# Optimization experiments

Hardware: AMD Instinct MI355X
Metric: run time of the kernel (lower is better)

The kernel has to match this reference:

```python
import jax, jax.numpy as jnp
import numpy as np

IO = 1024
D_SLOT = 128
SCALES = [1, 2, 4]
N = 4          # lcm of scales (streams / period)
K = 3          # number of scales (active slots per step)
S = 7          # sum of scales (total slots)
D = D_SLOT * S # 896, per-stream dim
H = K * N      # 12 heads
RANK = 256
HID = 3584
B, T = 4, 1024
EPS = 1e-5


def _tables():
    # active_slots[phase, scale_idx] -> slot id
    act = np.zeros((N, K), dtype=np.int32)
    for p in range(N):
        off = 0
        for i, s in enumerate(SCALES):
            act[p, i] = off + p % s
            off += s
    # head_assignments[stream, slot] -> head id (SHARED mode)
    ha = np.zeros((N, S), dtype=np.int32)
    off = 0
    for i, s in enumerate(SCALES):
        alpha = N // s
        for j in range(s):
            ha[:, off + j] = i * N + (np.arange(N) + alpha * j) % N
        off += s
    return act, ha

ACTIVE_SLOTS, HEAD_ASSIGN = _tables()


def layernorm(x, g, b):
    m = jnp.mean(x, axis=-1, keepdims=True)
    v = jnp.mean(jnp.square(x - m), axis=-1, keepdims=True)
    return (x - m) * jax.lax.rsqrt(v + EPS) * g + b


def setup_inputs() -> dict:
    key = jax.random.key(0)
    ks = jax.random.split(key, 16)
    f32 = jnp.float32
    return {
        'x': jax.random.normal(ks[0], (B, T, IO), f32),
        't': 3,
        'enc_base_w': jax.random.normal(ks[1], (D, IO), f32) * 0.02,
        'enc_A_w': jax.random.normal(ks[2], (RANK, IO), f32) * 0.02,
        'enc_B': jax.random.normal(ks[3], (RANK, N, D), f32) * 0.02,
        'enc_beta': jnp.asarray(0.01, f32),
        'ln_mixer_g': jnp.ones((D,), f32),
        'ln_mixer_b': jnp.zeros((D,), f32),
        'mix_w1': jax.random.normal(ks[4], (HID, D), f32) * 0.02,
        'mix_b1': jnp.zeros((HID,), f32),
        'mix_w2': jax.random.normal(ks[5], (D, HID), f32) * 0.02,
        'mix_b2': jnp.zeros((D,), f32),
        'ln_attn_g': jnp.ones((D,), f32),
        'ln_attn_b': jnp.zeros((D,), f32),
        'Wq': jax.random.normal(ks[6], (H, D, D_SLOT), f32) * 0.02,
        'Wk': jax.random.normal(ks[7], (H, D, D_SLOT), f32) * 0.02,
        'Wv': jax.random.normal(ks[8], (H, D, D_SLOT), f32) * 0.02,
        'dec_ln_g': jnp.ones((N * D,), f32),
        'dec_ln_b': jnp.zeros((N * D,), f32),
        'dec_down_w': jax.random.normal(ks[9], (RANK, N * D), f32) * 0.02,
        'dec_up_w': jax.random.normal(ks[10], (IO, RANK), f32) * 0.02,
    }


def reference(x, t, enc_base_w, enc_A_w, enc_B, enc_beta,
              ln_mixer_g, ln_mixer_b, mix_w1, mix_b1, mix_w2, mix_b2,
              ln_attn_g, ln_attn_b, Wq, Wk, Wv,
              dec_ln_g, dec_ln_b, dec_down_w, dec_up_w):
    b, tt, _ = x.shape
    # --- StreamLoRAEncoder: x [B,T,IO] -> z [B,T,N,D] ---
    base = x @ enc_base_w.T                       # [B,T,D]
    h = x @ enc_A_w.T                             # [B,T,RANK]
    delta = jnp.einsum('btr,rnd->btnd', h, enc_B) # [B,T,N,D]
    z = base[:, :, None, :] + enc_beta * delta

    # --- step(z, t, is_causal=True) ---
    phase = int(t) % N
    active = ACTIVE_SLOTS[phase]                               # [K]
    head_ids = HEAD_ASSIGN[np.arange(N)[:, None], active[None, :]]  # [N,K]

    # mixer (pre-LN MLP residual)
    zm = layernorm(z, ln_mixer_g, ln_mixer_b)
    m = jax.nn.gelu(zm @ mix_w1.T + mix_b1, approximate=False) @ mix_w2.T + mix_b2
    z_head = z + m                                             # [B,T,N,D]

    # per-head multi-scale attention; head input scope = STREAM (full D)
    hin = layernorm(z_head, ln_attn_g, ln_attn_b)              # [B,T,N,D]
    Wq_s, Wk_s, Wv_s = Wq[head_ids], Wk[head_ids], Wv[head_ids]  # [N,K,D,d]
    q = jnp.einsum('btnc,nkcd->btnkd', hin, Wq_s)
    k = jnp.einsum('btnc,nkcd->btnkd', hin, Wk_s)
    v = jnp.einsum('btnc,nkcd->btnkd', hin, Wv_s)
    scale = 1.0 / jnp.sqrt(jnp.asarray(D_SLOT, q.dtype))
    scores = jnp.einsum('bqnkd,bpnkd->bnkqp', q, k) * scale    # [B,N,K,T,T]
    causal = jnp.tril(jnp.ones((tt, tt), dtype=bool))
    scores = jnp.where(causal, scores, jnp.finfo(scores.dtype).min)
    attn = jax.nn.softmax(scores, axis=-1)
    out = jnp.einsum('bnkqp,bpnkd->bqnkd', attn, v)            # [B,T,N,K,d]

    # write attention outputs back into the active slots (residual)
    z_slots = z_head.reshape(b, tt, N, S, D_SLOT)
    z_new = z_slots.at[:, :, :, jnp.asarray(active), :].add(out)
    z_new = z_new.reshape(b, tt, N, D)

    # --- StreamLoRADecoder: z [B,T,N,D] -> y [B,T,IO] ---
    cat = z_new.reshape(b, tt, N * D)
    c = layernorm(cat, dec_ln_g, dec_ln_b)
    y = (c @ dec_down_w.T) @ dec_up_w.T
    return y
```

## Files before the change

### kernel.cpp

```cpp
#include <hip/hip_runtime.h>
#include <hip/hip_bf16.h>
#include <math.h>

typedef __hip_bfloat16 bf16;
typedef __attribute__((ext_vector_type(8))) short v8s;
typedef __attribute__((ext_vector_type(4))) float v4f;

#define EPI_F32    0
#define EPI_BF16   1
#define EPI_GELU   2
#define EPI_RESID  3
#define EPI_BCAST4 4
#define EPI_AXPY   5
#define EPI_RESID0 6

__device__ __forceinline__ float bf_lo(unsigned int w) { return __uint_as_float(w << 16); }
__device__ __forceinline__ float bf_hi(unsigned int w) { return __uint_as_float(w & 0xffff0000u); }
__device__ __forceinline__ unsigned short f2b_bits(float f) {
  unsigned int u = __float_as_uint(f);
  unsigned int r = (u + 0x7fffu + ((u >> 16) & 1u)) >> 16;
  return (unsigned short)r;
}
__device__ __forceinline__ void unpack8(uint4 u, float* f) {
  unsigned int w0 = u.x, w1 = u.y, w2 = u.z, w3 = u.w;
  f[0] = bf_lo(w0); f[1] = bf_hi(w0);
  f[2] = bf_lo(w1); f[3] = bf_hi(w1);
  f[4] = bf_lo(w2); f[5] = bf_hi(w2);
  f[6] = bf_lo(w3); f[7] = bf_hi(w3);
}
__device__ __forceinline__ void load8(const float* p, float* f) {
  float4 a = ((const float4*)p)[0];
  float4 b = ((const float4*)p)[1];
  f[0] = a.x; f[1] = a.y; f[2] = a.z; f[3] = a.w;
  f[4] = b.x; f[5] = b.y; f[6] = b.z; f[7] = b.w;
}

__global__ __launch_bounds__(256) void cvt_kernel(const float* __restrict__ src,
                                                  bf16* __restrict__ dst, int n)
{
  int i = (blockIdx.x * 256 + threadIdx.x) * 8;
  if (i >= n) return;
  float f[8]; load8(src + i, f);
  unsigned short us[8];
#pragma unroll
  for (int j = 0; j < 8; j++) us[j] = f2b_bits(f[j]);
  *(uint4*)((unsigned short*)dst + i) = *(uint4*)us;
}

__global__ __launch_bounds__(256) void cvt_t_kernel(const float* __restrict__ src,
                                                    bf16* __restrict__ dst, int R, int C)
{
  __shared__ float tile[32][33];
  const int c0 = blockIdx.x * 32, r0 = blockIdx.y * 32;
  const size_t bo = (size_t)blockIdx.z * R * C;
  const int tx = threadIdx.x & 31, ty = threadIdx.x >> 5;
#pragma unroll
  for (int i = 0; i < 4; i++) {
    int r = ty * 4 + i;
    tile[r][tx] = src[bo + (size_t)(r0 + r) * C + c0 + tx];
  }
  __syncthreads();
#pragma unroll
  for (int i = 0; i < 4; i++) {
    int r = ty * 4 + i;
    *((unsigned short*)dst + bo + (size_t)(c0 + r) * R + r0 + tx) = f2b_bits(tile[tx][r]);
  }
}

__global__ __launch_bounds__(256) void vt_kernel(const bf16* __restrict__ v,
                                                 bf16* __restrict__ vt)
{
  __shared__ float tile[64][65];
  const int h = blockIdx.z;
  const int t0 = blockIdx.x * 64, d0 = blockIdx.y * 64;
  const bf16* src = v + (size_t)h * 4096 * 128;
  bf16* dst = vt + (size_t)h * 128 * 4096;
  const int tid = threadIdx.x;
#pragma unroll
  for (int tt = 0; tt < 2; tt++) {
    int s = tt * 256 + tid;
    int r = s >> 3, c0 = (s & 7) * 8;
    float f[8];
    uint4 u = *(const uint4*)(src + (size_t)(t0 + r) * 128 + d0 + c0);
    unpack8(u, f);
#pragma unroll
    for (int j = 0; j < 8; j++) tile[r][c0 + j] = f[j];
  }
  __syncthreads();
#pragma unroll
  for (int tt = 0; tt < 2; tt++) {
    int s = tt * 256 + tid;
    int dr = s >> 3, c0 = (s & 7) * 8;
    unsigned short us[8];
#pragma unroll
    for (int j = 0; j < 8; j++) us[j] = f2b_bits(tile[c0 + j][dr]);
    *(uint4*)((unsigned short*)dst + (size_t)(d0 + dr) * 4096 + t0 + c0) = *(uint4*)us;
  }
}

__device__ __forceinline__ void stage_tile(const bf16* __restrict__ src, int ld, int r0, int k0,
                                           bf16* lds, int tid)
{
#pragma unroll
  for (int t = 0; t < 2; t++) {
    int s = t * 256 + tid;
    int m = s >> 2, c = s & 3;
    uint4 u = *(const uint4*)(src + (size_t)(r0 + m) * ld + k0 + c * 8);
    *(uint4*)&lds[m * 40 + c * 8] = u;
  }
}
__device__ __forceinline__ void stage_tile(const float* __restrict__ src, int ld, int r0, int k0,
                                           bf16* lds, int tid)
{
#pragma unroll
  for (int t = 0; t < 2; t++) {
    int s = t * 256 + tid;
    int m = s >> 2, c = s & 3;
    float f[8]; load8(src + (size_t)(r0 + m) * ld + k0 + c * 8, f);
    unsigned short us[8];
#pragma unroll
    for (int j = 0; j < 8; j++) us[j] = f2b_bits(f[j]);
    *(uint4*)&lds[m * 40 + c * 8] = *(uint4*)us;
  }
}

template<typename TA, typename TB, int EPI>
__device__ void mfma_core(const TA* __restrict__ A, int lda,
                          const TB* __restrict__ B, int ldb,
                          void* __restrict__ C, int ldc,
                          const float* __restrict__ bias,
                          const float* __restrict__ beta_p,
                          int m0, int n0, int K)
{
  __shared__ bf16 As[128 * 40];
  __shared__ bf16 Bs[128 * 40];
  const int tid = threadIdx.x;
  const int lane = tid & 63, wave = tid >> 6;
  const int mw = (wave & 1) * 64, nw = (wave >> 1) * 64;
  const int row = lane & 15, kc = lane >> 4;

  v4f acc[4][4];
  const v4f vzero = {0.f, 0.f, 0.f, 0.f};
#pragma unroll
  for (int i = 0; i < 4; i++)
#pragma unroll
    for (int j = 0; j < 4; j++) acc[i][j] = vzero;

  for (int k0 = 0; k0 < K; k0 += 32) {
    stage_tile(A, lda, m0, k0, As, tid);
    stage_tile(B, ldb, n0, k0, Bs, tid);
    __syncthreads();
    v8s af[4], bfr[4];
#pragma unroll
    for (int i = 0; i < 4; i++)
      af[i] = *(const v8s*)&As[(mw + i * 16 + row) * 40 + kc * 8];
#pragma unroll
    for (int j = 0; j < 4; j++)
      bfr[j] = *(const v8s*)&Bs[(nw + j * 16 + row) * 40 + kc * 8];
#pragma unroll
    for (int i = 0; i < 4; i++)
#pragma unroll
      for (int j = 0; j < 4; j++)
        acc[i][j] = __builtin_amdgcn_mfma_f32_16x16x32_bf16(af[i], bfr[j], acc[i][j], 0, 0, 0);
    __syncthreads();
  }

  const int cl = lane & 15, rq = lane >> 4;
  const float beta = (EPI == EPI_AXPY) ? beta_p[0] : 0.f;
#pragma unroll
  for (int mi = 0; mi < 4; mi++) {
#pragma unroll
    for (int nj = 0; nj < 4; nj++) {
      const int col = n0 + nw + nj * 16 + cl;
#pragma unroll
      for (int i = 0; i < 4; i++) {
        const int r = m0 + mw + mi * 16 + rq * 4 + i;
        float v = acc[mi][nj][i];
        if (EPI == EPI_F32) {
          ((float*)C)[(size_t)r * ldc + col] = v;
        } else if (EPI == EPI_BF16) {
          ((unsigned short*)C)[(size_t)r * ldc + col] = f2b_bits(v);
        } else if (EPI == EPI_GELU) {
          v += bias[col];
          v = 0.5f * v * (1.f + erff(v * 0.70710678118654752f));
          ((unsigned short*)C)[(size_t)r * ldc + col] = f2b_bits(v);
        } else if (EPI == EPI_RESID) {
          float* Z = (float*)C;
          size_t idx = (size_t)r * ldc + col;
          Z[idx] = Z[idx] + v + bias[col];
        } else if (EPI == EPI_RESID0) {
          float* Z = (float*)C;
          size_t idx = (size_t)r * ldc + col;
          Z[idx] = Z[idx] + v;
        } else if (EPI == EPI_BCAST4) {
          float* Z = (float*)C;
#pragma unroll
          for (int rep = 0; rep < 4; rep++)
            Z[(size_t)r * 3584 + rep * 896 + col] = v;
        } else if (EPI == EPI_AXPY) {
          float* Z = (float*)C;
          size_t idx = (size_t)r * 3584 + col;
          Z[idx] = Z[idx] + beta * v;
        }
      }
    }
  }
}

template<typename TA, typename TB, int EPI>
__global__ __launch_bounds__(256) void mfma_gemm(const TA* __restrict__ A, int lda,
                                                 const TB* __restrict__ B, int ldb,
                                                 void* __restrict__ C, int ldc,
                                                 const float* __restrict__ bias,
                                                 const float* __restrict__ beta_p, int K)
{
  mfma_core<TA, TB, EPI>(A, lda, B, ldb, C, ldc, bias, beta_p,
                         blockIdx.y * 128, blockIdx.x * 128, K);
}

__global__ __launch_bounds__(256) void qkv_mfma(const bf16* __restrict__ hin,
                                                const bf16* __restrict__ Wt,
                                                bf16* __restrict__ qkv,
                                                const int* __restrict__ tptr)
{
  const int zb = blockIdx.z;
  const int type = zb / 12, rem = zb % 12, n = rem / 3, kh = rem % 3;
  const int phase = ((tptr[0] % 4) + 4) % 4;
  const int hid = (kh == 0) ? n
                : (kh == 1) ? 4 + (n + 2 * (phase & 1)) % 4
                            : 8 + (n + phase) % 4;
  const bf16* B = Wt + ((size_t)type * 12 + hid) * 128 * 896;
  bf16* out = qkv + ((size_t)type * 12 + n * 3 + kh) * 4096 * 128;
  mfma_core<bf16, bf16, EPI_BF16>(hin + n * 896, 3584, B, 896, out, 128,
                                  nullptr, nullptr, blockIdx.y * 128, 0, 896);
}

__global__ __launch_bounds__(256) void ln_kernel(const float* __restrict__ in,
                                                 const float* __restrict__ g,
                                                 const float* __restrict__ bsh,
                                                 bf16* __restrict__ out, int D)
{
  __shared__ float row[3584];
  __shared__ float red[256];
  const int tid = threadIdx.x;
  const size_t base = (size_t)blockIdx.x * D;
  float s = 0.f;
  for (int i = tid; i < D; i += 256) { float v = in[base + i]; row[i] = v; s += v; }
  red[tid] = s; __syncthreads();
  for (int o = 128; o > 0; o >>= 1) { if (tid < o) red[tid] += red[tid + o]; __syncthreads(); }
  const float mean = red[0] / (float)D;
  __syncthreads();
  s = 0.f;
  for (int i = tid; i < D; i += 256) { float d = row[i] - mean; s += d * d; }
  red[tid] = s; __syncthreads();
  for (int o = 128; o > 0; o >>= 1) { if (tid < o) red[tid] += red[tid + o]; __syncthreads(); }
  const float inv = rsqrtf(red[0] / (float)D + 1e-5f);
  for (int i = tid; i < D; i += 256) {
    float v = (row[i] - mean) * inv * g[i] + bsh[i];
    *((unsigned short*)out + base + i) = f2b_bits(v);
  }
}

__global__ __launch_bounds__(256) void attn_mfma(const bf16* __restrict__ qkv,
                                                 const bf16* __restrict__ vt,
                                                 float* __restrict__ z,
                                                 const int* __restrict__ tptr)
{
  __shared__ bf16 Ks[64 * 136];
  __shared__ bf16 Vs[128 * 72];
  __shared__ bf16 Ps[4][16 * 72];
  const int tid = threadIdx.x;
  const int lane = tid & 63, wave = tid >> 6;
  const int cl = lane & 15, rq = lane >> 4;
  const int qb = 15 - blockIdx.x;
  const int bnk = blockIdx.y;
  const int b = bnk / 12, rem = bnk % 12, n = rem / 3, kh = rem % 3;
  const int phase = ((tptr[0] % 4) + 4) % 4;
  const int slot = (kh == 0) ? 0 : (kh == 1) ? 1 + (phase & 1) : 3 + phase;
  const int head = n * 3 + kh;
  const size_t HS = (size_t)12 * 4096 * 128;
  const bf16* qp = qkv + ((size_t)head * 4096 + b * 1024) * 128;
  const bf16* kp = qkv + HS + ((size_t)head * 4096 + b * 1024) * 128;
  const bf16* vtp = vt + (size_t)head * 128 * 4096;

  v8s aq[4];
  {
    const bf16* qrow = qp + (size_t)(qb * 64 + wave * 16 + cl) * 128 + rq * 8;
#pragma unroll
    for (int c = 0; c < 4; c++) aq[c] = *(const v8s*)(qrow + c * 32);
  }
  v4f oacc[8];
  const v4f vzero = {0.f, 0.f, 0.f, 0.f};
#pragma unroll
  for (int c = 0; c < 8; c++) oacc[c] = vzero;
  float m_i[4] = {-1e30f, -1e30f, -1e30f, -1e30f};
  float l_i[4] = {0.f, 0.f, 0.f, 0.f};

  for (int kt = 0; kt <= qb; kt++) {
    __syncthreads();
#pragma unroll
    for (int t = 0; t < 4; t++) {
      int s = t * 256 + tid;
      int r = s >> 4, c0 = (s & 15) * 8;
      *(uint4*)&Ks[r * 136 + c0] = *(const uint4*)(kp + (size_t)(kt * 64 + r) * 128 + c0);
    }
#pragma unroll
    for (int t = 0; t < 4; t++) {
      int s = t * 256 + tid;
      int d = s >> 3, c0 = (s & 7) * 8;
      *(uint4*)&Vs[d * 72 + c0] =
          *(const uint4*)(vtp + (size_t)d * 4096 + b * 1024 + kt * 64 + c0);
    }
    __syncthreads();

    v4f s_acc[4];
#pragma unroll
    for (int blk = 0; blk < 4; blk++) {
      s_acc[blk] = vzero;
#pragma unroll
      for (int c = 0; c < 4; c++) {
        v8s bk = *(const v8s*)&Ks[(blk * 16 + cl) * 136 + c * 32 + rq * 8];
        s_acc[blk] = __builtin_amdgcn_mfma_f32_16x16x32_bf16(aq[c], bk, s_acc[blk], 0, 0, 0);
      }
    }
#pragma unroll
    for (int blk = 0; blk < 4; blk++)
#pragma unroll
      for (int i = 0; i < 4; i++) {
        float sv = s_acc[blk][i] * 0.088388347648318447f;
        if (kt == qb && (blk * 16 + cl) > (wave * 16 + rq * 4 + i)) sv = -1e30f;
        s_acc[blk][i] = sv;
      }
    float al[4];
#pragma unroll
    for (int i = 0; i < 4; i++) {
      float mx = fmaxf(fmaxf(s_acc[0][i], s_acc[1][i]), fmaxf(s_acc[2][i], s_acc[3][i]));
      mx = fmaxf(mx, __shfl_xor(mx, 1, 64));
      mx = fmaxf(mx, __shfl_xor(mx, 2, 64));
      mx = fmaxf(mx, __shfl_xor(mx, 4, 64));
      mx = fmaxf(mx, __shfl_xor(mx, 8, 64));
      const float mn = fmaxf(m_i[i], mx);
      al[i] = __expf(m_i[i] - mn);
      m_i[i] = mn;
      float ps = 0.f;
#pragma unroll
      for (int blk = 0; blk < 4; blk++) {
        float p = __expf(s_acc[blk][i] - mn);
        s_acc[blk][i] = p;
        ps += p;
      }
      ps += __shfl_xor(ps, 1, 64);
      ps += __shfl_xor(ps, 2, 64);
      ps += __shfl_xor(ps, 4, 64);
      ps += __shfl_xor(ps, 8, 64);
      l_i[i] = l_i[i] * al[i] + ps;
    }
#pragma unroll
    for (int c = 0; c < 8; c++)
#pragma unroll
      for (int i = 0; i < 4; i++) oacc[c][i] *= al[i];
    bf16* ps = Ps[wave];
#pragma unroll
    for (int blk = 0; blk < 4; blk++)
#pragma unroll
      for (int i = 0; i < 4; i++)
        *((unsigned short*)ps + (rq * 4 + i) * 72 + blk * 16 + cl) = f2b_bits(s_acc[blk][i]);
    v8s pa[2];
#pragma unroll
    for (int c = 0; c < 2; c++)
      pa[c] = *(const v8s*)&ps[cl * 72 + c * 32 + rq * 8];
#pragma unroll
    for (int c = 0; c < 8; c++)
#pragma unroll
      for (int ch = 0; ch < 2; ch++) {
        v8s bv = *(const v8s*)&Vs[(c * 16 + cl) * 72 + ch * 32 + rq * 8];
        oacc[c] = __builtin_amdgcn_mfma_f32_16x16x32_bf16(pa[ch], bv, oacc[c], 0, 0, 0);
      }
  }
#pragma unroll
  for (int c = 0; c < 8; c++) {
    const int d = c * 16 + cl;
#pragma unroll
    for (int i = 0; i < 4; i++) {
      const int t = qb * 64 + wave * 16 + rq * 4 + i;
      float* dst = z + ((size_t)(b * 1024 + t)) * 3584 + n * 896 + slot * 128 + d;
      *dst += oacc[c][i] / l_i[i];
    }
  }
}

extern "C" void kernel_launch(void* const* d_in, const int* in_sizes, int n_in,
                              void* d_out, int out_size, void* d_ws, size_t ws_size,
                              hipStream_t stream)
{
  const float* x        = (const float*)d_in[0];
  const int*   tptr     = (const int*)d_in[1];
  const float* enc_base = (const float*)d_in[2];
  const float* enc_A    = (const float*)d_in[3];
  const float* enc_B    = (const float*)d_in[4];
  const float* beta_p   = (const float*)d_in[5];
  const float* lnm_g    = (const float*)d_in[6];
  const float* lnm_b    = (const float*)d_in[7];
  const float* w1       = (const float*)d_in[8];
  const float* b1       = (const float*)d_in[9];
  const float* w2       = (const float*)d_in[10];
  const float* b2       = (const float*)d_in[11];
  const float* lna_g    = (const float*)d_in[12];
  const float* lna_b    = (const float*)d_in[13];
  const float* Wq       = (const float*)d_in[14];
  const float* Wk       = (const float*)d_in[15];
  const float* Wv       = (const float*)d_in[16];
  const float* dln_g    = (const float*)d_in[17];
  const float* dln_b    = (const float*)d_in[18];
  const float* down_w   = (const float*)d_in[19];
  const float* up_w     = (const float*)d_in[20];

  const bool big = (ws_size >= (size_t)228458496);
  char* ws = (char*)d_ws;
  float* z = (float*)ws;
  bf16 *hbuf, *act, *qkv, *bufb, *w1b, *w2b, *encBt, *Wt;
  if (big) {
    hbuf  = (bf16*)(ws + (size_t)58720256);
    act   = (bf16*)(ws + (size_t)58720256);
    qkv   = (bf16*)(ws + (size_t)58720256);
    bufb  = (bf16*)(ws + (size_t)176160768);
    w1b   = (bf16*)(ws + (size_t)205520896);
    w2b   = (bf16*)(ws + (size_t)211943424);
    encBt = (bf16*)(ws + (size_t)218365952);
    Wt    = (bf16*)(ws + (size_t)220200960);
  } else {
    hbuf  = (bf16*)(ws + (size_t)58720256);
    act   = (bf16*)(ws + (size_t)58720256);
    qkv   = (bf16*)(ws + (size_t)58720256);
    bufb  = (bf16*)(ws + (size_t)96468992);
    w1b   = (bf16*)(ws + (size_t)125829120);
    w2b   = (bf16*)(ws + (size_t)132251648);
    encBt = (bf16*)(ws + (size_t)138674176);
    Wt    = (bf16*)(ws + (size_t)140509184);
  }

  dim3 blk(256);
  cvt_kernel<<<1568, blk, 0, stream>>>(w1, w1b, 3211264);
  cvt_kernel<<<1568, blk, 0, stream>>>(w2, w2b, 3211264);
  cvt_t_kernel<<<dim3(112, 8, 1), blk, 0, stream>>>(enc_B, encBt, 256, 3584);
  cvt_t_kernel<<<dim3(4, 28, 12), blk, 0, stream>>>(Wq, Wt,                      896, 128);
  cvt_t_kernel<<<dim3(4, 28, 12), blk, 0, stream>>>(Wk, Wt + (size_t)12*128*896, 896, 128);
  cvt_t_kernel<<<dim3(4, 28, 12), blk, 0, stream>>>(Wv, Wt + (size_t)24*128*896, 896, 128);

  mfma_gemm<float, float, EPI_BCAST4><<<dim3(7, 32), blk, 0, stream>>>(x, 1024, enc_base, 1024, z, 0, nullptr, nullptr, 1024);
  mfma_gemm<float, float, EPI_BF16><<<dim3(2, 32), blk, 0, stream>>>(x, 1024, enc_A, 1024, hbuf, 256, nullptr, nullptr, 1024);
  mfma_gemm<bf16, bf16, EPI_AXPY><<<dim3(28, 32), blk, 0, stream>>>(hbuf, 256, encBt, 256, z, 3584, nullptr, beta_p, 256);
  ln_kernel<<<dim3(16384), blk, 0, stream>>>(z, lnm_g, lnm_b, bufb, 896);

  if (big) {
    mfma_gemm<bf16, bf16, EPI_GELU><<<dim3(28, 128), blk, 0, stream>>>(bufb, 896, w1b, 896, act, 3584, b1, nullptr, 896);
    mfma_gemm<bf16, bf16, EPI_RESID><<<dim3(7, 128), blk, 0, stream>>>(act, 3584, w2b, 3584, z, 896, b2, nullptr, 3584);
  } else {
    for (int c = 0; c < 4; c++) {
      mfma_gemm<bf16, bf16, EPI_GELU><<<dim3(7, 128), blk, 0, stream>>>(
          bufb, 896, w1b + (size_t)c * 896 * 896, 896, act, 896, b1 + c * 896, nullptr, 896);
      if (c == 0)
        mfma_gemm<bf16, bf16, EPI_RESID><<<dim3(7, 128), blk, 0, stream>>>(
            act, 896, w2b + (size_t)c * 896, 3584, z, 896, b2, nullptr, 896);
      else
        mfma_gemm<bf16, bf16, EPI_RESID0><<<dim3(7, 128), blk, 0, stream>>>(
            act, 896, w2b + (size_t)c * 896, 3584, z, 896, nullptr, nullptr, 896);
    }
  }

  ln_kernel<<<dim3(16384), blk, 0, stream>>>(z, lna_g, lna_b, bufb, 896);
  qkv_mfma<<<dim3(1, 32, 36), blk, 0, stream>>>(bufb, Wt, qkv, tptr);
  vt_kernel<<<dim3(64, 2, 12), blk, 0, stream>>>(qkv + (size_t)24 * 4096 * 128, bufb);
  attn_mfma<<<dim3(16, 48), blk, 0, stream>>>(qkv, bufb, z, tptr);
  ln_kernel<<<dim3(4096), blk, 0, stream>>>(z, dln_g, dln_b, bufb, 3584);
  mfma_gemm<bf16, float, EPI_BF16><<<dim3(2, 32), blk, 0, stream>>>(bufb, 3584, down_w, 3584, hbuf, 256, nullptr, nullptr, 3584);
  mfma_gemm<bf16, float, EPI_F32><<<dim3(8, 32), blk, 0, stream>>>(hbuf, 256, up_w, 256, (float*)d_out, 1024, nullptr, nullptr, 256);
}
```

Measured before the change: 1.059 ms.

## Use direct global-to-LDS loads for bf16 tiles and swizzle block order

Staging of bf16 GEMM operands now uses global_load_lds, which writes straight into LDS and bypasses registers. Because of this the LDS row pitch shrinks from 40 to 32 elements, with no padding. The MLP GEMMs also launch as a 1D grid whose block index is remapped so that consecutive blocks spread across the M dimension, aiming for better L2 reuse of weights. Dropping the padding may bring back LDS bank conflicts on fragment reads. There is also no explicit vmcnt wait before the barrier, which risks a correctness or ordering dependence on the compiler's waitcnt insertion.

```diff
diff --git a/kernel.cpp b/kernel.cpp
--- a/kernel.cpp
+++ b/kernel.cpp
@@ -34,6 +34,11 @@
   f[0] = a.x; f[1] = a.y; f[2] = a.z; f[3] = a.w;
   f[4] = b.x; f[5] = b.y; f[6] = b.z; f[7] = b.w;
 }
+__device__ __forceinline__ void gl_lds16(const void* g, void* l) {
+  __builtin_amdgcn_global_load_lds(
+      (__attribute__((address_space(1))) void*)g,
+      (__attribute__((address_space(3))) void*)l, 16, 0, 0);
+}
 
 __global__ __launch_bounds__(256) void cvt_kernel(const float* __restrict__ src,
                                                   bf16* __restrict__ dst, int n)
@@ -98,18 +103,17 @@
   }
 }
 
-__device__ __forceinline__ void stage_tile(const bf16* __restrict__ src, int ld, int r0, int k0,
-                                           bf16* lds, int tid)
+__device__ __forceinline__ void stage_async(const bf16* __restrict__ src, int ld, int r0, int k0,
+                                            bf16* lds, int wave, int lane)
 {
 #pragma unroll
   for (int t = 0; t < 2; t++) {
-    int s = t * 256 + tid;
-    int m = s >> 2, c = s & 3;
-    uint4 u = *(const uint4*)(src + (size_t)(r0 + m) * ld + k0 + c * 8);
-    *(uint4*)&lds[m * 40 + c * 8] = u;
-  }
-}
-__device__ __forceinline__ void stage_tile(const float* __restrict__ src, int ld, int r0, int k0,
+    int seg = wave * 2 + t;
+    const bf16* g = src + (size_t)(r0 + seg * 16 + (lane >> 2)) * ld + k0 + (lane & 3) * 8;
+    gl_lds16(g, lds + seg * 512);
+  }
+}
+__device__ __forceinline__ void stage_sync(const float* __restrict__ src, int ld, int r0, int k0,
                                            bf16* lds, int tid)
 {
 #pragma unroll
@@ -120,9 +124,15 @@
     unsigned short us[8];
 #pragma unroll
     for (int j = 0; j < 8; j++) us[j] = f2b_bits(f[j]);
-    *(uint4*)&lds[m * 40 + c * 8] = *(uint4*)us;
-  }
-}
+    *(uint4*)&lds[m * 32 + c * 8] = *(uint4*)us;
+  }
+}
+__device__ __forceinline__ void stage_tile(const bf16* __restrict__ src, int ld, int r0, int k0,
+                                           bf16* lds, int tid, int wave, int lane)
+{ stage_async(src, ld, r0, k0, lds, wave, lane); }
+__device__ __forceinline__ void stage_tile(const float* __restrict__ src, int ld, int r0, int k0,
+                                           bf16* lds, int tid, int wave, int lane)
+{ stage_sync(src, ld, r0, k0, lds, tid); }
 
 template<typename TA, typename TB, int EPI>
 __device__ void mfma_core(const TA* __restrict__ A, int lda,
@@ -132,8 +142,8 @@
                           const float* __restrict__ beta_p,
                           int m0, int n0, int K)
 {
-  __shared__ bf16 As[128 * 40];
-  __shared__ bf16 Bs[128 * 40];
+  __shared__ bf16 As[128 * 32];
+  __shared__ bf16 Bs[128 * 32];
   const int tid = threadIdx.x;
   const int lane = tid & 63, wave = tid >> 6;
   const int mw = (wave & 1) * 64, nw = (wave >> 1) * 64;
@@ -147,16 +157,16 @@
     for (int j = 0; j < 4; j++) acc[i][j] = vzero;
 
   for (int k0 = 0; k0 < K; k0 += 32) {
-    stage_tile(A, lda, m0, k0, As, tid);
-    stage_tile(B, ldb, n0, k0, Bs, tid);
+    stage_tile(A, lda, m0, k0, As, tid, wave, lane);
+    stage_tile(B, ldb, n0, k0, Bs, tid, wave, lane);
     __syncthreads();
     v8s af[4], bfr[4];
 #pragma unroll
     for (int i = 0; i < 4; i++)
-      af[i] = *(const v8s*)&As[(mw + i * 16 + row) * 40 + kc * 8];
+      af[i] = *(const v8s*)&As[(mw + i * 16 + row) * 32 + kc * 8];
 #pragma unroll
     for (int j = 0; j < 4; j++)
-      bfr[j] = *(const v8s*)&Bs[(nw + j * 16 + row) * 40 + kc * 8];
+      bfr[j] = *(const v8s*)&Bs[(nw + j * 16 + row) * 32 + kc * 8];
 #pragma unroll
     for (int i = 0; i < 4; i++)
 #pragma unroll
@@ -216,6 +226,19 @@
 {
   mfma_core<TA, TB, EPI>(A, lda, B, ldb, C, ldc, bias, beta_p,
                          blockIdx.y * 128, blockIdx.x * 128, K);
+}
+
+template<typename TA, typename TB, int EPI>
+__global__ __launch_bounds__(256) void mfma_gemm_sw(const TA* __restrict__ A, int lda,
+                                                    const TB* __restrict__ B, int ldb,
+                                                    void* __restrict__ C, int ldc,
+                                                    const float* __restrict__ bias,
+                                                    const float* __restrict__ beta_p, int K)
+{
+  const int lin = blockIdx.x;
+  const int m0 = ((((lin & 7) << 4) | ((lin >> 3) & 15))) * 128;
+  const int n0 = (lin >> 7) * 128;
+  mfma_core<TA, TB, EPI>(A, lda, B, ldb, C, ldc, bias, beta_p, m0, n0, K);
 }
 
 __global__ __launch_bounds__(256) void qkv_mfma(const bf16* __restrict__ hin,
@@ -453,17 +476,17 @@
   ln_kernel<<<dim3(16384), blk, 0, stream>>>(z, lnm_g, lnm_b, bufb, 896);
 
   if (big) {
-    mfma_gemm<bf16, bf16, EPI_GELU><<<dim3(28, 128), blk, 0, stream>>>(bufb, 896, w1b, 896, act, 3584, b1, nullptr, 896);
-    mfma_gemm<bf16, bf16, EPI_RESID><<<dim3(7, 128), blk, 0, stream>>>(act, 3584, w2b, 3584, z, 896, b2, nullptr, 3584);
+    mfma_gemm_sw<bf16, bf16, EPI_GELU><<<dim3(3584), blk, 0, stream>>>(bufb, 896, w1b, 896, act, 3584, b1, nullptr, 896);
+    mfma_gemm_sw<bf16, bf16, EPI_RESID><<<dim3(896), blk, 0, stream>>>(act, 3584, w2b, 3584, z, 896, b2, nullptr, 3584);
   } else {
     for (int c = 0; c < 4; c++) {
-      mfma_gemm<bf16, bf16, EPI_GELU><<<dim3(7, 128), blk, 0, stream>>>(
+      mfma_gemm_sw<bf16, bf16, EPI_GELU><<<dim3(896), blk, 0, stream>>>(
           bufb, 896, w1b + (size_t)c * 896 * 896, 896, act, 896, b1 + c * 896, nullptr, 896);
       if (c == 0)
-        mfma_gemm<bf16, bf16, EPI_RESID><<<dim3(7, 128), blk, 0, stream>>>(
+        mfma_gemm_sw<bf16, bf16, EPI_RESID><<<dim3(896), blk, 0, stream>>>(
             act, 896, w2b + (size_t)c * 896, 3584, z, 896, b2, nullptr, 896);
       else
-        mfma_gemm<bf16, bf16, EPI_RESID0><<<dim3(7, 128), blk, 0, stream>>>(
+        mfma_gemm_sw<bf16, bf16, EPI_RESID0><<<dim3(896), blk, 0, stream>>>(
             act, 896, w2b + (size_t)c * 896, 3584, z, 896, nullptr, nullptr, 896);
     }
   }
```

Result: faster. 1.023 ms (-3.4%).
